# Optimization experiments

Hardware: AMD Instinct MI355X
Metric: run time of the kernel (lower is better)

Reference implementation:

```python
import jax, jax.numpy as jnp
import numpy as np

B, QL, KL = 2, 1024, 4096
H = 1024          # hidden_size
NH = 16           # num_heads
HD = H // NH      # head_dim = 64


def setup_inputs() -> dict:
    key = jax.random.key(0)
    k1, k2, k3, k4, k5 = jax.random.split(key, 5)
    s = 1.0 / np.sqrt(H)
    return {
        "query": jax.random.normal(k1, (B, QL, H), dtype=jnp.float32),
        "key_value": jax.random.normal(k2, (B, KL, H), dtype=jnp.float32),
        "w_q": jax.random.uniform(k3, (H, H), dtype=jnp.float32, minval=-s, maxval=s),
        "w_kv": jax.random.uniform(k4, (H, 2 * H), dtype=jnp.float32, minval=-s, maxval=s),
        "w_out": jax.random.uniform(k5, (H, H), dtype=jnp.float32, minval=-s, maxval=s),
    }


def reference(query, key_value, w_q, w_kv, w_out):
    # projections
    q = (query @ w_q).reshape(B, QL, NH, HD).transpose(0, 2, 1, 3)      # [B,NH,QL,HD]
    kv = (key_value @ w_kv).reshape(B, KL, 2, NH, HD)
    k = kv[:, :, 0].transpose(0, 2, 1, 3)                               # [B,NH,KL,HD]
    v = kv[:, :, 1].transpose(0, 2, 1, 3)                               # [B,NH,KL,HD]
    # scaled dot-product attention (explicit, matching source)
    scale = 1.0 / np.sqrt(HD).astype(np.float32)
    attn = jnp.einsum("bhqd,bhkd->bhqk", q, k) * scale                  # [B,NH,QL,KL]
    attn = jax.nn.softmax(attn, axis=-1)
    out = jnp.einsum("bhqk,bhkd->bhqd", attn, v)                        # [B,NH,QL,HD]
    out = out.transpose(0, 2, 1, 3).reshape(B, QL, H)
    return out @ w_out
```

## Files before the change

kernel.cpp:

```cpp
#include <hip/hip_runtime.h>

#define Bb   2
#define QL   1024
#define KL   4096
#define Hh   1024
#define NH   16
#define HD   64

#define KSPLIT 2
#define CHUNK  (KL / KSPLIT)
#define NTT    (CHUNK / 64)

typedef unsigned short u16;
typedef __attribute__((ext_vector_type(8))) short bf16x8;
typedef __attribute__((ext_vector_type(4))) float f32x4;
typedef __attribute__((ext_vector_type(16))) float f32x16;

#define QSCALE 0.1803368801111204f
#define RTHR   11.0f

__device__ __forceinline__ u16 f2bf(float f) {
    union { float f; unsigned int u; } v; v.f = f;
    unsigned int r = (v.u + 0x7FFFu + ((v.u >> 16) & 1u)) >> 16;
    return (u16)r;
}

__device__ __forceinline__ unsigned int cvt_pk_bf16(float lo, float hi) {
    unsigned int r;
    asm("v_cvt_pk_bf16_f32 %0, %1, %2" : "=v"(r) : "v"(lo), "v"(hi));
    return r;
}

__device__ __forceinline__ float max3f(float a, float b, float c) {
    float r;
    asm("v_max3_f32 %0, %1, %2, %3" : "=v"(r) : "v"(a), "v"(b), "v"(c));
    return r;
}

__device__ __forceinline__ void plane32swap(unsigned int& a, unsigned int& b) {
    asm volatile("v_permlane32_swap_b32 %0, %1" : "+v"(a), "+v"(b));
}

__device__ __forceinline__ void gload16(const void* g, void* l) {
    __builtin_amdgcn_global_load_lds(
        (const __attribute__((address_space(1))) void*)g,
        (__attribute__((address_space(3))) void*)l, 16, 0, 0);
}

__device__ __forceinline__ uint4 pack8(const float4& f0, const float4& f1) {
    uint4 o;
    o.x = cvt_pk_bf16(f0.x, f0.y);
    o.y = cvt_pk_bf16(f0.z, f0.w);
    o.z = cvt_pk_bf16(f1.x, f1.y);
    o.w = cvt_pk_bf16(f1.z, f1.w);
    return o;
}

__global__ __launch_bounds__(256) void prep_all(const float* __restrict__ wq,
                                                const float* __restrict__ wkv,
                                                const float* __restrict__ wout,
                                                const float* __restrict__ qact,
                                                const float* __restrict__ kvact,
                                                u16* __restrict__ wqT,
                                                u16* __restrict__ wkvT,
                                                u16* __restrict__ woutT,
                                                u16* __restrict__ qb,
                                                u16* __restrict__ kvb) {
    __shared__ float T[64][65];
    int bid = blockIdx.x;
    if (bid >= 1024) {
        bid -= 1024;
        const float* in; u16* out;
        if (bid < 1024) { in = qact;  out = qb;  }
        else            { in = kvact; out = kvb; bid -= 1024; }
        const size_t i = ((size_t)bid * 256 + threadIdx.x) * 8;
        float4 f0 = *reinterpret_cast<const float4*>(in + i);
        float4 f1 = *reinterpret_cast<const float4*>(in + i + 4);
        *reinterpret_cast<uint4*>(out + i) = pack8(f0, f1);
        return;
    }
    const float* in; u16* out; int C;
    if (bid < 256)      { in = wq;   out = wqT;   C = 1024; }
    else if (bid < 768) { in = wkv;  out = wkvT;  C = 2048; bid -= 256; }
    else                { in = wout; out = woutT; C = 1024; bid -= 768; }
    const int nc = C >> 6;
    const int c0 = (bid % nc) * 64;
    const int r0 = (bid / nc) * 64;
    const int t  = threadIdx.x;
    const int tx = t & 15, ty = t >> 4;
#pragma unroll
    for (int p = 0; p < 4; ++p) {
        const int r = ty + p * 16;
        float4 v = *reinterpret_cast<const float4*>(in + (size_t)(r0 + r) * C + c0 + tx * 4);
        T[r][tx * 4 + 0] = v.x; T[r][tx * 4 + 1] = v.y;
        T[r][tx * 4 + 2] = v.z; T[r][tx * 4 + 3] = v.w;
    }
    __syncthreads();
#pragma unroll
    for (int p = 0; p < 4; ++p) {
        const int c = ty + p * 16;
        const int n = c0 + c;
        ushort4 o;
        o.x = f2bf(T[tx * 4 + 0][c]); o.y = f2bf(T[tx * 4 + 1][c]);
        o.z = f2bf(T[tx * 4 + 2][c]); o.w = f2bf(T[tx * 4 + 3][c]);
        const int kb   = r0 + tx * 4;
        const int kout = (kb & ~63) | ((((kb >> 3) & 7) ^ (n & 7)) << 3) | (kb & 7);
        *reinterpret_cast<ushort4*>(out + (size_t)n * 1024 + kout) = o;
    }
}

__global__ __launch_bounds__(256) void qkvgemm(const u16* __restrict__ Aq,
                                               const u16* __restrict__ Akv,
                                               const u16* __restrict__ wqT,
                                               const u16* __restrict__ wkvT,
                                               u16* __restrict__ Qb,
                                               u16* __restrict__ KT,
                                               u16* __restrict__ VT) {
    __shared__ u16 As[128 * 64];
    __shared__ u16 Bs[128 * 64];
    const int tid = threadIdx.x, lane = tid & 63, w = tid >> 6;
    const int wr = w >> 1, wc = w & 1;
    const int x7 = lane & 7;
    const int lrow = lane >> 3, lcol = (lane & 7) * 8;
    const int swcol = lcol ^ ((lrow & 7) << 3);

    if (blockIdx.x < 1024) {
        const int id = blockIdx.x;
        const int sw = (id & 7) * 128 + (id >> 3);
        const int bx = sw % 16, by = sw / 16;
        const int row0 = by * 128, col0 = bx * 128;
        const int MROW = wr * 64;

        f32x4 acc[4][4];
#pragma unroll
        for (int m = 0; m < 4; ++m)
#pragma unroll
            for (int n = 0; n < 4; ++n) acc[m][n] = (f32x4){0.f, 0.f, 0.f, 0.f};

        auto stage = [&](int k0) {
            __syncthreads();
#pragma unroll
            for (int p = 0; p < 4; ++p) {
                const int base = w * 512 + p * 2048;
                const int row  = (base >> 6) + lrow;
                gload16(Akv + (size_t)(row0 + row) * 1024 + k0 + swcol, &As[base]);
                gload16(wkvT + (size_t)(col0 + row) * 1024 + k0 + lcol, &Bs[base]);
            }
            __syncthreads();
        };

        if (col0 < 1024) {
            for (int k0 = 0; k0 < 1024; k0 += 64) {
                stage(k0);
#pragma unroll
                for (int kk = 0; kk < 2; ++kk) {
                    bf16x8 af[4], bfr[4];
                    const int G = ((kk * 4 + (lane >> 4)) ^ x7) * 8;
#pragma unroll
                    for (int m = 0; m < 4; ++m)
                        af[m] = *reinterpret_cast<const bf16x8*>(
                            &As[(MROW + m * 16 + (lane & 15)) * 64 + G]);
#pragma unroll
                    for (int n = 0; n < 4; ++n)
                        bfr[n] = *reinterpret_cast<const bf16x8*>(
                            &Bs[(wc * 64 + n * 16 + (lane & 15)) * 64 + G]);
#pragma unroll
                    for (int m = 0; m < 4; ++m)
#pragma unroll
                        for (int n = 0; n < 4; ++n)
                            acc[m][n] = __builtin_amdgcn_mfma_f32_16x16x32_bf16(
                                bfr[n], af[m], acc[m][n], 0, 0, 0);
                }
            }
#pragma unroll
            for (int m = 0; m < 4; ++m) {
                const int gr  = row0 + MROW + m * 16 + (lane & 15);
                const int b   = gr >> 12;
                const int k   = gr & 4095;
                const int kt_i = k >> 6, k_in = k & 63;
#pragma unroll
                for (int n = 0; n < 4; ++n) {
                    const int gc0 = col0 + wc * 64 + n * 16 + (lane >> 4) * 4;
                    const int h   = gc0 >> 6, d0 = gc0 & 63;
                    u16* blob = KT + (((size_t)((b << 4) + h) * 64 + kt_i) << 9) * 8;
                    const int og = k_in * 8 + ((d0 >> 3) ^ (k_in & 7));
                    ushort4 pk;
                    pk.x = f2bf(acc[m][n][0]); pk.y = f2bf(acc[m][n][1]);
                    pk.z = f2bf(acc[m][n][2]); pk.w = f2bf(acc[m][n][3]);
                    *reinterpret_cast<ushort4*>(&blob[og * 8 + (d0 & 7)]) = pk;
                }
            }
        } else {
            for (int k0 = 0; k0 < 1024; k0 += 64) {
                stage(k0);
#pragma unroll
                for (int kk = 0; kk < 2; ++kk) {
                    bf16x8 af[4], bfr[4];
                    const int G = ((kk * 4 + (lane >> 4)) ^ x7) * 8;
#pragma unroll
                    for (int m = 0; m < 4; ++m)
                        af[m] = *reinterpret_cast<const bf16x8*>(
                            &As[(MROW + m * 16 + (lane & 15)) * 64 + G]);
#pragma unroll
                    for (int n = 0; n < 4; ++n)
                        bfr[n] = *reinterpret_cast<const bf16x8*>(
                            &Bs[(wc * 64 + n * 16 + (lane & 15)) * 64 + G]);
#pragma unroll
                    for (int m = 0; m < 4; ++m)
#pragma unroll
                        for (int n = 0; n < 4; ++n)
                            acc[m][n] = __builtin_amdgcn_mfma_f32_16x16x32_bf16(
                                af[m], bfr[n], acc[m][n], 0, 0, 0);
                }
            }
#pragma unroll
            for (int m = 0; m < 4; ++m) {
                const int gr0 = row0 + MROW + m * 16 + (lane >> 4) * 4;
                const int b   = gr0 >> 12;
                const int k   = gr0 & 4095;
                const int kt_i = k >> 6, k_in = k & 63;
#pragma unroll
                for (int n = 0; n < 4; ++n) {
                    const int gc = col0 + wc * 64 + n * 16 + (lane & 15);
                    const int h  = (gc & 1023) >> 6, d = gc & 63;
                    u16* blob = VT + (((size_t)((b << 4) + h) * 64 + kt_i) << 9) * 8;
                    const int og = d * 8 + ((k_in >> 3) ^ (d & 7));
                    ushort4 pk;
                    pk.x = f2bf(acc[m][n][0]); pk.y = f2bf(acc[m][n][1]);
                    pk.z = f2bf(acc[m][n][2]); pk.w = f2bf(acc[m][n][3]);
                    *reinterpret_cast<ushort4*>(&blob[og * 8 + (k_in & 7)]) = pk;
                }
            }
        }
    } else {
        const int id = blockIdx.x - 1024;
        const int sw = (id & 7) * 32 + (id >> 3);
        const int bx = sw % 8, by = sw / 8;
        const int row0 = by * 64, col0 = bx * 128;
        const int MROW = wr * 32;

        f32x4 acc[2][4];
#pragma unroll
        for (int m = 0; m < 2; ++m)
#pragma unroll
            for (int n = 0; n < 4; ++n) acc[m][n] = (f32x4){0.f, 0.f, 0.f, 0.f};

        for (int k0 = 0; k0 < 1024; k0 += 64) {
            __syncthreads();
#pragma unroll
            for (int p = 0; p < 2; ++p) {
                const int base = w * 512 + p * 2048;
                const int row  = (base >> 6) + lrow;
                gload16(Aq + (size_t)(row0 + row) * 1024 + k0 + swcol, &As[base]);
            }
#pragma unroll
            for (int p = 0; p < 4; ++p) {
                const int base = w * 512 + p * 2048;
                const int row  = (base >> 6) + lrow;
                gload16(wqT + (size_t)(col0 + row) * 1024 + k0 + lcol, &Bs[base]);
            }
            __syncthreads();
#pragma unroll
            for (int kk = 0; kk < 2; ++kk) {
                bf16x8 af[2], bfr[4];
                const int G = ((kk * 4 + (lane >> 4)) ^ x7) * 8;
#pragma unroll
                for (int m = 0; m < 2; ++m)
                    af[m] = *reinterpret_cast<const bf16x8*>(
                        &As[(MROW + m * 16 + (lane & 15)) * 64 + G]);
#pragma unroll
                for (int n = 0; n < 4; ++n)
                    bfr[n] = *reinterpret_cast<const bf16x8*>(
                        &Bs[(wc * 64 + n * 16 + (lane & 15)) * 64 + G]);
#pragma unroll
                for (int m = 0; m < 2; ++m)
#pragma unroll
                    for (int n = 0; n < 4; ++n)
                        acc[m][n] = __builtin_amdgcn_mfma_f32_16x16x32_bf16(
                            af[m], bfr[n], acc[m][n], 0, 0, 0);
            }
        }
#pragma unroll
        for (int m = 0; m < 2; ++m)
#pragma unroll
            for (int n = 0; n < 4; ++n) {
                const int gc = col0 + wc * 64 + n * 16 + (lane & 15);
#pragma unroll
                for (int r = 0; r < 4; ++r) {
                    const int gr = row0 + MROW + m * 16 + (lane >> 4) * 4 + r;
                    Qb[(size_t)gr * 1024 + gc] = f2bf(acc[m][n][r] * QSCALE);
                }
            }
    }
}

__global__ __launch_bounds__(256, 2) void attn_mfma(const u16* __restrict__ Qb,
                                                    const u16* __restrict__ KT,
                                                    const u16* __restrict__ VT2,
                                                    float* __restrict__ Op,
                                                    float* __restrict__ m_ws,
                                                    float* __restrict__ l_ws) {
    __shared__ u16 Ks[2][4096];
    __shared__ u16 Vs[2][4096];

    const int bid0 = blockIdx.x;
    const int bid  = (bid0 & 7) * 64 + (bid0 >> 3);
    const int qb   = bid & 7;
    const int h    = (bid >> 3) & 15;
    const int b    = (bid >> 7) & 1;
    const int c    = bid >> 8;
    const int tid  = threadIdx.x;
    const int lane = tid & 63;
    const int w    = tid >> 6;
    const int q    = lane & 31;
    const int hl   = lane >> 5;
    const int l7   = lane & 7;
    const int q0   = qb * 128;
    const int bh   = b * NH + h;

    bf16x8 qa[4];
    {
        const u16* qsrc = Qb + (size_t)(b * QL + q0 + w * 32 + q) * Hh
                          + h * HD + hl * 8;
#pragma unroll
        for (int dc = 0; dc < 4; ++dc)
            qa[dc] = *reinterpret_cast<const bf16x8*>(qsrc + dc * 16);
    }
    asm volatile("s_waitcnt vmcnt(0)" ::: "memory");

    float m_i = -1e30f, l_i = 0.f;
    f32x16 accO[2];
#pragma unroll
    for (int d2 = 0; d2 < 2; ++d2)
#pragma unroll
        for (int r = 0; r < 16; ++r) accO[d2][r] = 0.f;

    const u16* Kb0 = &Ks[0][q * 64];
    const u16* Vb0 = &Vs[0][q * 64];
    int off[4];
#pragma unroll
    for (int j = 0; j < 4; ++j) off[j] = (((j * 2 + hl) ^ l7) << 3);

    const size_t tb0 = ((size_t)bh * 64 + c * NTT) * 4096;
    const u16* kpt = KT  + tb0 + (size_t)(w * 64 + lane) * 8 + 1024;
    const u16* vpt = VT2 + tb0 + (size_t)(w * 64 + lane) * 8 + 1024;
    u16* kdst[2] = { &Ks[0][w * 512], &Ks[1][w * 512] };
    u16* vdst[2] = { &Vs[0][w * 512], &Vs[1][w * 512] };

    gload16(kpt - 1024, kdst[0]);
    gload16(kpt + 1024, kdst[0] + 2048);
    gload16(vpt - 1024, vdst[0]);
    gload16(vpt + 1024, vdst[0] + 2048);

    auto tile = [&](int CUR, int t) {
        __builtin_amdgcn_s_barrier();
        if (t + 1 < NTT) {
            kpt += 4096; vpt += 4096;
            gload16(kpt - 1024, kdst[CUR ^ 1]);
            gload16(kpt + 1024, kdst[CUR ^ 1] + 2048);
            gload16(vpt - 1024, vdst[CUR ^ 1]);
            gload16(vpt + 1024, vdst[CUR ^ 1] + 2048);
            asm volatile("s_waitcnt vmcnt(4)" ::: "memory");
        } else {
            asm volatile("s_waitcnt vmcnt(0)" ::: "memory");
        }
        __builtin_amdgcn_sched_barrier(0);
        __builtin_amdgcn_s_barrier();

        f32x16 sc[2];
        __builtin_amdgcn_s_setprio(1);
#pragma unroll
        for (int kc = 0; kc < 2; ++kc) {
            f32x16 z;
#pragma unroll
            for (int r = 0; r < 16; ++r) z[r] = 0.f;
#pragma unroll
            for (int dc = 0; dc < 4; ++dc) {
                bf16x8 kf = *reinterpret_cast<const bf16x8*>(
                    Kb0 + CUR * 4096 + kc * 2048 + off[dc]);
                z = __builtin_amdgcn_mfma_f32_32x32x16_bf16(kf, qa[dc], z, 0, 0, 0);
            }
            sc[kc] = z;
        }
        __builtin_amdgcn_s_setprio(0);

        float mx = max3f(sc[0][0], sc[0][1], sc[0][2]);
#pragma unroll
        for (int i = 3; i + 1 < 32; i += 2)
            mx = max3f(mx, sc[i >> 4][i & 15], sc[(i + 1) >> 4][(i + 1) & 15]);
        mx = fmaxf(mx, sc[1][15]);
        mx = fmaxf(mx, __shfl_xor(mx, 32));

        if (__any(mx > m_i + RTHR)) {
            const float mnew = fmaxf(m_i, mx);
            const float al   = exp2f(m_i - mnew);
            m_i = mnew;
            l_i *= al;
#pragma unroll
            for (int d2 = 0; d2 < 2; ++d2)
#pragma unroll
                for (int r = 0; r < 16; ++r) accO[d2][r] *= al;
        }
#pragma unroll
        for (int kc = 0; kc < 2; ++kc)
#pragma unroll
            for (int r = 0; r < 16; ++r) sc[kc][r] = exp2f(sc[kc][r] - m_i);

        {
            float p0 = sc[0][0], p1 = sc[0][1], p2 = sc[0][2], p3 = sc[0][3];
#pragma unroll
            for (int i = 4; i < 16; i += 4) {
                p0 += sc[0][i];     p1 += sc[0][i + 1];
                p2 += sc[0][i + 2]; p3 += sc[0][i + 3];
            }
#pragma unroll
            for (int i = 0; i < 16; i += 4) {
                p0 += sc[1][i];     p1 += sc[1][i + 1];
                p2 += sc[1][i + 2]; p3 += sc[1][i + 3];
            }
            float sum = (p0 + p1) + (p2 + p3);
            sum += __shfl_xor(sum, 32);
            l_i += sum;
        }

        __builtin_amdgcn_s_setprio(1);
#pragma unroll
        for (int kk = 0; kk < 4; ++kk) {
            const int kc  = kk >> 1;
            const int rb  = (kk & 1) * 8;
            unsigned int X0 = cvt_pk_bf16(sc[kc][rb + 0], sc[kc][rb + 1]);
            unsigned int X1 = cvt_pk_bf16(sc[kc][rb + 2], sc[kc][rb + 3]);
            unsigned int Y0 = cvt_pk_bf16(sc[kc][rb + 4], sc[kc][rb + 5]);
            unsigned int Y1 = cvt_pk_bf16(sc[kc][rb + 6], sc[kc][rb + 7]);
            plane32swap(X0, Y0);
            plane32swap(X1, Y1);
            uint4 wv = make_uint4(X0, X1, Y0, Y1);
            bf16x8 pf;
            __builtin_memcpy(&pf, &wv, 16);
            bf16x8 vf0 = *reinterpret_cast<const bf16x8*>(
                Vb0 + CUR * 4096 + off[kk]);
            bf16x8 vf1 = *reinterpret_cast<const bf16x8*>(
                Vb0 + CUR * 4096 + 2048 + off[kk]);
            accO[0] = __builtin_amdgcn_mfma_f32_32x32x16_bf16(vf0, pf, accO[0], 0, 0, 0);
            accO[1] = __builtin_amdgcn_mfma_f32_32x32x16_bf16(vf1, pf, accO[1], 0, 0, 0);
        }
        __builtin_amdgcn_s_setprio(0);
    };

    for (int t = 0; t < NTT; t += 2) {
        tile(0, t);
        tile(1, t + 1);
    }

    float* opc = Op + (size_t)c * ((size_t)Bb * QL * Hh)
                 + (size_t)(b * QL + q0 + w * 32 + q) * Hh + h * HD;
#pragma unroll
    for (int d2 = 0; d2 < 2; ++d2) {
#pragma unroll
        for (int b2 = 0; b2 < 4; ++b2) {
            float4 v = make_float4(accO[d2][4 * b2 + 0], accO[d2][4 * b2 + 1],
                                   accO[d2][4 * b2 + 2], accO[d2][4 * b2 + 3]);
            *reinterpret_cast<float4*>(opc + d2 * 32 + b2 * 8 + hl * 4) = v;
        }
    }
    if (hl == 0) {
        const int idx = ((c * Bb + b) * NH + h) * QL + q0 + w * 32 + q;
        m_ws[idx] = m_i;
        l_ws[idx] = l_i;
    }
}

__global__ __launch_bounds__(256) void attn_combine(const float* __restrict__ Op,
                                                    const float* __restrict__ m_ws,
                                                    const float* __restrict__ l_ws,
                                                    u16* __restrict__ AO) {
    const int id  = blockIdx.x * 256 + threadIdx.x;
    const int e0  = id * 4;
    const int row = e0 >> 10;
    const int col = e0 & 1023;
    const int b   = row >> 10;
    const int q   = row & 1023;
    const int hh  = col >> 6;
    const int i0  = ((b << 4) + hh) * 1024 + q;
    const int i1  = i0 + 32768;
    const float m0 = m_ws[i0], m1 = m_ws[i1];
    const float l0 = l_ws[i0], l1 = l_ws[i1];
    const float ms = fmaxf(m0, m1);
    const float w0 = exp2f(m0 - ms), w1 = exp2f(m1 - ms);
    const float inv = 1.f / (l0 * w0 + l1 * w1);
    const size_t off = (size_t)row * 1024 + col;
    float4 o0 = *reinterpret_cast<const float4*>(Op + off);
    float4 o1 = *reinterpret_cast<const float4*>(Op + (size_t)Bb * QL * Hh + off);
    ushort4 o;
    o.x = f2bf((o0.x * w0 + o1.x * w1) * inv);
    o.y = f2bf((o0.y * w0 + o1.y * w1) * inv);
    o.z = f2bf((o0.z * w0 + o1.z * w1) * inv);
    o.w = f2bf((o0.w * w0 + o1.w * w1) * inv);
    *reinterpret_cast<ushort4*>(AO + off) = o;
}

__global__ __launch_bounds__(256) void ogemm(const u16* __restrict__ AO,
                                             const u16* __restrict__ Bt,
                                             float* __restrict__ C) {
    __shared__ u16 As[64 * 64];
    __shared__ u16 Bs[128 * 64];
    const int nwg = gridDim.x * gridDim.y;
    const int id  = blockIdx.y * gridDim.x + blockIdx.x;
    const int sw  = (id & 7) * (nwg >> 3) + (id >> 3);
    const int bx  = sw % gridDim.x, by = sw / gridDim.x;
    const int tid = threadIdx.x, lane = tid & 63, w = tid >> 6;
    const int wr = w >> 1, wc = w & 1;
    const int row0 = by * 64, col0 = bx * 128;
    const int MROW = wr * 32;
    const int x7   = lane & 7;
    const int lrow = lane >> 3, lcol = (lane & 7) * 8;
    const int swcol = lcol ^ ((lrow & 7) << 3);

    f32x4 acc[2][4];
#pragma unroll
    for (int m = 0; m < 2; ++m)
#pragma unroll
        for (int n = 0; n < 4; ++n) acc[m][n] = (f32x4){0.f, 0.f, 0.f, 0.f};

    for (int k0 = 0; k0 < 1024; k0 += 64) {
        __syncthreads();
#pragma unroll
        for (int p = 0; p < 2; ++p) {
            const int base = w * 512 + p * 2048;
            const int row  = (base >> 6) + lrow;
            gload16(AO + (size_t)(row0 + row) * 1024 + k0 + swcol, &As[base]);
        }
#pragma unroll
        for (int p = 0; p < 4; ++p) {
            const int base = w * 512 + p * 2048;
            const int row  = (base >> 6) + lrow;
            gload16(Bt + (size_t)(col0 + row) * 1024 + k0 + lcol, &Bs[base]);
        }
        __syncthreads();
#pragma unroll
        for (int kk = 0; kk < 2; ++kk) {
            bf16x8 af[2], bfr[4];
            const int G = ((kk * 4 + (lane >> 4)) ^ x7) * 8;
#pragma unroll
            for (int m = 0; m < 2; ++m)
                af[m] = *reinterpret_cast<const bf16x8*>(
                    &As[(MROW + m * 16 + (lane & 15)) * 64 + G]);
#pragma unroll
            for (int n = 0; n < 4; ++n)
                bfr[n] = *reinterpret_cast<const bf16x8*>(
                    &Bs[(wc * 64 + n * 16 + (lane & 15)) * 64 + G]);
#pragma unroll
            for (int m = 0; m < 2; ++m)
#pragma unroll
                for (int n = 0; n < 4; ++n)
                    acc[m][n] = __builtin_amdgcn_mfma_f32_16x16x32_bf16(
                        af[m], bfr[n], acc[m][n], 0, 0, 0);
        }
    }
#pragma unroll
    for (int m = 0; m < 2; ++m)
#pragma unroll
        for (int n = 0; n < 4; ++n) {
            const int gc = col0 + wc * 64 + n * 16 + (lane & 15);
#pragma unroll
            for (int r = 0; r < 4; ++r) {
                const int gr = row0 + MROW + m * 16 + (lane >> 4) * 4 + r;
                C[(size_t)gr * 1024 + gc] = acc[m][n][r];
            }
        }
}

extern "C" void kernel_launch(void* const* d_in, const int* in_sizes, int n_in,
                              void* d_out, int out_size, void* d_ws, size_t ws_size,
                              hipStream_t stream) {
    const float* query     = (const float*)d_in[0];
    const float* key_value = (const float*)d_in[1];
    const float* w_q       = (const float*)d_in[2];
    const float* w_kv      = (const float*)d_in[3];
    const float* w_out     = (const float*)d_in[4];
    float* out = (float*)d_out;

    char* ws = (char*)d_ws;
    const size_t MB = 1024 * 1024;
    u16*   KT    = (u16*)(ws);
    u16*   VT    = (u16*)(ws + 16 * MB);
    u16*   kvbf  = (u16*)(ws + 32 * MB);
    float* Opart = (float*)(ws + 32 * MB);
    u16*   Qb    = (u16*)(ws + 48 * MB);
    u16*   wkvT  = (u16*)(ws + 52 * MB);
    u16*   wqT   = (u16*)(ws + 56 * MB);
    u16*   woutT = (u16*)(ws + 58 * MB);
    float* m_wsp = (float*)(ws + 60 * MB);
    float* l_wsp = (float*)(ws + 60 * MB + 256 * 1024);
    u16*   qbf   = (u16*)(ws + 64 * MB);
    u16*   AO    = (u16*)(ws + 64 * MB);

    dim3 blk(256);

    prep_all<<<6144, blk, 0, stream>>>(w_q, w_kv, w_out, query, key_value,
                                       wqT, wkvT, woutT, qbf, kvbf);

    qkvgemm<<<1280, blk, 0, stream>>>(qbf, kvbf, wqT, wkvT, Qb, KT, VT);

    attn_mfma<<<dim3(KSPLIT * 256), blk, 0, stream>>>(
        Qb, KT, VT, Opart, m_wsp, l_wsp);

    attn_combine<<<2048, blk, 0, stream>>>(Opart, m_wsp, l_wsp, AO);

    ogemm<<<dim3(8, 32), blk, 0, stream>>>(AO, woutT, out);
}
```

Before: 150.5 us.

## Double-buffer LDS tiles in projection and output GEMMs to overlap loads with MFMA

```diff
diff --git a/kernel.cpp b/kernel.cpp
--- a/kernel.cpp
+++ b/kernel.cpp
@@ -116,8 +116,8 @@
                                                u16* __restrict__ Qb,
                                                u16* __restrict__ KT,
                                                u16* __restrict__ VT) {
-    __shared__ u16 As[128 * 64];
-    __shared__ u16 Bs[128 * 64];
+    __shared__ u16 As[2 * 8192];
+    __shared__ u16 Bs[2 * 8192];
     const int tid = threadIdx.x, lane = tid & 63, w = tid >> 6;
     const int wr = w >> 1, wc = w & 1;
     const int x7 = lane & 7;
@@ -137,41 +137,67 @@
 #pragma unroll
             for (int n = 0; n < 4; ++n) acc[m][n] = (f32x4){0.f, 0.f, 0.f, 0.f};
 
-        auto stage = [&](int k0) {
-            __syncthreads();
+        auto issue = [&](int k0, int bufi) {
 #pragma unroll
             for (int p = 0; p < 4; ++p) {
-                const int base = w * 512 + p * 2048;
-                const int row  = (base >> 6) + lrow;
-                gload16(Akv + (size_t)(row0 + row) * 1024 + k0 + swcol, &As[base]);
-                gload16(wkvT + (size_t)(col0 + row) * 1024 + k0 + lcol, &Bs[base]);
-            }
-            __syncthreads();
+                const int off  = w * 512 + p * 2048;
+                const int row  = (off >> 6) + lrow;
+                gload16(Akv + (size_t)(row0 + row) * 1024 + k0 + swcol,
+                        &As[bufi * 8192 + off]);
+                gload16(wkvT + (size_t)(col0 + row) * 1024 + k0 + lcol,
+                        &Bs[bufi * 8192 + off]);
+            }
         };
 
-        if (col0 < 1024) {
-            for (int k0 = 0; k0 < 1024; k0 += 64) {
-                stage(k0);
-#pragma unroll
-                for (int kk = 0; kk < 2; ++kk) {
-                    bf16x8 af[4], bfr[4];
-                    const int G = ((kk * 4 + (lane >> 4)) ^ x7) * 8;
-#pragma unroll
-                    for (int m = 0; m < 4; ++m)
-                        af[m] = *reinterpret_cast<const bf16x8*>(
-                            &As[(MROW + m * 16 + (lane & 15)) * 64 + G]);
-#pragma unroll
-                    for (int n = 0; n < 4; ++n)
-                        bfr[n] = *reinterpret_cast<const bf16x8*>(
-                            &Bs[(wc * 64 + n * 16 + (lane & 15)) * 64 + G]);
+        issue(0, 0);
+        const bool kmode = (col0 < 1024);
+
+        auto step = [&](int CUR, int t) {
+            __builtin_amdgcn_s_barrier();
+            if (t + 1 < 16) {
+                issue((t + 1) * 64, CUR ^ 1);
+                asm volatile("s_waitcnt vmcnt(8)" ::: "memory");
+            } else {
+                asm volatile("s_waitcnt vmcnt(0)" ::: "memory");
+            }
+            __builtin_amdgcn_sched_barrier(0);
+            __builtin_amdgcn_s_barrier();
+#pragma unroll
+            for (int kk = 0; kk < 2; ++kk) {
+                bf16x8 af[4], bfr[4];
+                const int G = ((kk * 4 + (lane >> 4)) ^ x7) * 8;
+#pragma unroll
+                for (int m = 0; m < 4; ++m)
+                    af[m] = *reinterpret_cast<const bf16x8*>(
+                        &As[CUR * 8192 + (MROW + m * 16 + (lane & 15)) * 64 + G]);
+#pragma unroll
+                for (int n = 0; n < 4; ++n)
+                    bfr[n] = *reinterpret_cast<const bf16x8*>(
+                        &Bs[CUR * 8192 + (wc * 64 + n * 16 + (lane & 15)) * 64 + G]);
+                if (kmode) {
 #pragma unroll
                     for (int m = 0; m < 4; ++m)
 #pragma unroll
                         for (int n = 0; n < 4; ++n)
                             acc[m][n] = __builtin_amdgcn_mfma_f32_16x16x32_bf16(
                                 bfr[n], af[m], acc[m][n], 0, 0, 0);
+                } else {
+#pragma unroll
+                    for (int m = 0; m < 4; ++m)
+#pragma unroll
+                        for (int n = 0; n < 4; ++n)
+                            acc[m][n] = __builtin_amdgcn_mfma_f32_16x16x32_bf16(
+                                af[m], bfr[n], acc[m][n], 0, 0, 0);
                 }
             }
+        };
+
+        for (int t = 0; t < 16; t += 2) {
+            step(0, t);
+            step(1, t + 1);
+        }
+
+        if (kmode) {
 #pragma unroll
             for (int m = 0; m < 4; ++m) {
                 const int gr  = row0 + MROW + m * 16 + (lane & 15);
@@ -191,28 +217,6 @@
                 }
             }
         } else {
-            for (int k0 = 0; k0 < 1024; k0 += 64) {
-                stage(k0);
-#pragma unroll
-                for (int kk = 0; kk < 2; ++kk) {
-                    bf16x8 af[4], bfr[4];
-                    const int G = ((kk * 4 + (lane >> 4)) ^ x7) * 8;
-#pragma unroll
-                    for (int m = 0; m < 4; ++m)
-                        af[m] = *reinterpret_cast<const bf16x8*>(
-                            &As[(MROW + m * 16 + (lane & 15)) * 64 + G]);
-#pragma unroll
-                    for (int n = 0; n < 4; ++n)
-                        bfr[n] = *reinterpret_cast<const bf16x8*>(
-                            &Bs[(wc * 64 + n * 16 + (lane & 15)) * 64 + G]);
-#pragma unroll
-                    for (int m = 0; m < 4; ++m)
-#pragma unroll
-                        for (int n = 0; n < 4; ++n)
-                            acc[m][n] = __builtin_amdgcn_mfma_f32_16x16x32_bf16(
-                                af[m], bfr[n], acc[m][n], 0, 0, 0);
-                }
-            }
 #pragma unroll
             for (int m = 0; m < 4; ++m) {
                 const int gr0 = row0 + MROW + m * 16 + (lane >> 4) * 4;
@@ -245,21 +249,35 @@
 #pragma unroll
             for (int n = 0; n < 4; ++n) acc[m][n] = (f32x4){0.f, 0.f, 0.f, 0.f};
 
-        for (int k0 = 0; k0 < 1024; k0 += 64) {
-            __syncthreads();
+        auto issue = [&](int k0, int bufi) {
 #pragma unroll
             for (int p = 0; p < 2; ++p) {
-                const int base = w * 512 + p * 2048;
-                const int row  = (base >> 6) + lrow;
-                gload16(Aq + (size_t)(row0 + row) * 1024 + k0 + swcol, &As[base]);
+                const int off  = w * 512 + p * 2048;
+                const int row  = (off >> 6) + lrow;
+                gload16(Aq + (size_t)(row0 + row) * 1024 + k0 + swcol,
+                        &As[bufi * 8192 + off]);
             }
 #pragma unroll
             for (int p = 0; p < 4; ++p) {
-                const int base = w * 512 + p * 2048;
-                const int row  = (base >> 6) + lrow;
-                gload16(wqT + (size_t)(col0 + row) * 1024 + k0 + lcol, &Bs[base]);
-            }
-            __syncthreads();
+                const int off  = w * 512 + p * 2048;
+                const int row  = (off >> 6) + lrow;
+                gload16(wqT + (size_t)(col0 + row) * 1024 + k0 + lcol,
+                        &Bs[bufi * 8192 + off]);
+            }
+        };
+
+        issue(0, 0);
+
+        auto step = [&](int CUR, int t) {
+            __builtin_amdgcn_s_barrier();
+            if (t + 1 < 16) {
+                issue((t + 1) * 64, CUR ^ 1);
+                asm volatile("s_waitcnt vmcnt(6)" ::: "memory");
+            } else {
+                asm volatile("s_waitcnt vmcnt(0)" ::: "memory");
+            }
+            __builtin_amdgcn_sched_barrier(0);
+            __builtin_amdgcn_s_barrier();
 #pragma unroll
             for (int kk = 0; kk < 2; ++kk) {
                 bf16x8 af[2], bfr[4];
@@ -267,11 +285,11 @@
 #pragma unroll
                 for (int m = 0; m < 2; ++m)
                     af[m] = *reinterpret_cast<const bf16x8*>(
-                        &As[(MROW + m * 16 + (lane & 15)) * 64 + G]);
+                        &As[CUR * 8192 + (MROW + m * 16 + (lane & 15)) * 64 + G]);
 #pragma unroll
                 for (int n = 0; n < 4; ++n)
                     bfr[n] = *reinterpret_cast<const bf16x8*>(
-                        &Bs[(wc * 64 + n * 16 + (lane & 15)) * 64 + G]);
+                        &Bs[CUR * 8192 + (wc * 64 + n * 16 + (lane & 15)) * 64 + G]);
 #pragma unroll
                 for (int m = 0; m < 2; ++m)
 #pragma unroll
@@ -279,7 +297,13 @@
                         acc[m][n] = __builtin_amdgcn_mfma_f32_16x16x32_bf16(
                             af[m], bfr[n], acc[m][n], 0, 0, 0);
             }
-        }
+        };
+
+        for (int t = 0; t < 16; t += 2) {
+            step(0, t);
+            step(1, t + 1);
+        }
+
 #pragma unroll
         for (int m = 0; m < 2; ++m)
 #pragma unroll
@@ -502,8 +526,8 @@
 __global__ __launch_bounds__(256) void ogemm(const u16* __restrict__ AO,
                                              const u16* __restrict__ Bt,
                                              float* __restrict__ C) {
-    __shared__ u16 As[64 * 64];
-    __shared__ u16 Bs[128 * 64];
+    __shared__ u16 As[2 * 4096];
+    __shared__ u16 Bs[2 * 8192];
     const int nwg = gridDim.x * gridDim.y;
     const int id  = blockIdx.y * gridDim.x + blockIdx.x;
     const int sw  = (id & 7) * (nwg >> 3) + (id >> 3);
@@ -522,21 +546,35 @@
 #pragma unroll
         for (int n = 0; n < 4; ++n) acc[m][n] = (f32x4){0.f, 0.f, 0.f, 0.f};
 
-    for (int k0 = 0; k0 < 1024; k0 += 64) {
-        __syncthreads();
+    auto issue = [&](int k0, int bufi) {
 #pragma unroll
         for (int p = 0; p < 2; ++p) {
-            const int base = w * 512 + p * 2048;
-            const int row  = (base >> 6) + lrow;
-            gload16(AO + (size_t)(row0 + row) * 1024 + k0 + swcol, &As[base]);
+            const int off  = w * 512 + p * 2048;
+            const int row  = (off >> 6) + lrow;
+            gload16(AO + (size_t)(row0 + row) * 1024 + k0 + swcol,
+                    &As[bufi * 4096 + off]);
         }
 #pragma unroll
         for (int p = 0; p < 4; ++p) {
-            const int base = w * 512 + p * 2048;
-            const int row  = (base >> 6) + lrow;
-            gload16(Bt + (size_t)(col0 + row) * 1024 + k0 + lcol, &Bs[base]);
-        }
-        __syncthreads();
+            const int off  = w * 512 + p * 2048;
+            const int row  = (off >> 6) + lrow;
+            gload16(Bt + (size_t)(col0 + row) * 1024 + k0 + lcol,
+                    &Bs[bufi * 8192 + off]);
+        }
+    };
+
+    issue(0, 0);
+
+    auto step = [&](int CUR, int t) {
+        __builtin_amdgcn_s_barrier();
+        if (t + 1 < 16) {
+            issue((t + 1) * 64, CUR ^ 1);
+            asm volatile("s_waitcnt vmcnt(6)" ::: "memory");
+        } else {
+            asm volatile("s_waitcnt vmcnt(0)" ::: "memory");
+        }
+        __builtin_amdgcn_sched_barrier(0);
+        __builtin_amdgcn_s_barrier();
 #pragma unroll
         for (int kk = 0; kk < 2; ++kk) {
             bf16x8 af[2], bfr[4];
@@ -544,11 +582,11 @@
 #pragma unroll
             for (int m = 0; m < 2; ++m)
                 af[m] = *reinterpret_cast<const bf16x8*>(
-                    &As[(MROW + m * 16 + (lane & 15)) * 64 + G]);
+                    &As[CUR * 4096 + (MROW + m * 16 + (lane & 15)) * 64 + G]);
 #pragma unroll
             for (int n = 0; n < 4; ++n)
                 bfr[n] = *reinterpret_cast<const bf16x8*>(
-                    &Bs[(wc * 64 + n * 16 + (lane & 15)) * 64 + G]);
+                    &Bs[CUR * 8192 + (wc * 64 + n * 16 + (lane & 15)) * 64 + G]);
 #pragma unroll
             for (int m = 0; m < 2; ++m)
 #pragma unroll
@@ -556,7 +594,13 @@
                     acc[m][n] = __builtin_amdgcn_mfma_f32_16x16x32_bf16(
                         af[m], bfr[n], acc[m][n], 0, 0, 0);
         }
-    }
+    };
+
+    for (int t = 0; t < 16; t += 2) {
+        step(0, t);
+        step(1, t + 1);
+    }
+
 #pragma unroll
     for (int m = 0; m < 2; ++m)
 #pragma unroll
```

Result: slower. 169.6 us (+12.7%).
